# Kernel tuning notes

Measured on AMD Instinct MI355X. Metric: run time of the kernel, lower is better.

## Reference

```python
import jax, jax.numpy as jnp
import numpy as np
from jax import lax

LRELU_SLOPE = 0.2
GAIN = 2.0 ** 0.5
EPS = 1e-8


def setup_inputs() -> dict:
    key = jax.random.key(0)
    ks = jax.random.split(key, 8)
    B, NDW, CIN, COUT, H, W = 4, 512, 16, 16, 1024, 1024
    return {
        "w": jax.random.normal(ks[0], (B, NDW), jnp.float32),
        "x": jax.random.normal(ks[1], (B, CIN, H, W), jnp.float32),
        "noise": jax.random.normal(ks[2], (B, 1, H, W), jnp.float32),
        "fc_weight": jax.random.normal(ks[3], (CIN, NDW), jnp.float32),
        "fc_bias": jnp.ones((CIN,), jnp.float32),
        "conv_weight": jax.random.normal(ks[4], (COUT, CIN, 3, 3), jnp.float32),
        "conv_bias": jax.random.normal(ks[5], (COUT,), jnp.float32),
        "scale_noise": jnp.float32(0.1),
    }


def reference(w, x, noise, fc_weight, fc_bias, conv_weight, conv_bias, scale_noise):
    NDW = fc_weight.shape[1]
    COUT, CIN, KH, KW = conv_weight.shape
    # equal_lr scaling (FC): weight * n_dim_in**-0.5
    s = w @ (fc_weight.T * (NDW ** -0.5)) + fc_bias  # [B, CIN] style per input channel
    # equal_lr scaling (Conv): weight * (in_channels * k^2)**-0.5
    wc = conv_weight * ((CIN * KH * KW) ** -0.5)  # [COUT, CIN, 3, 3]
    # demodulation coefficient: d[b,o] = 1/sqrt(sum_{i,kh,kw} (s[b,i]*wc[o,i,kh,kw])^2 + eps)
    w2 = (wc ** 2).sum(axis=(2, 3))  # [COUT, CIN]
    d = lax.rsqrt((s ** 2) @ w2.T + EPS)  # [B, COUT]
    # modulate input instead of materializing per-sample weights (mathematically identical)
    xm = x * s[:, :, None, None]
    y = lax.conv_general_dilated(
        xm, wc, window_strides=(1, 1), padding=((1, 1), (1, 1)),
        dimension_numbers=("NCHW", "OIHW", "NCHW"))
    y = y * d[:, :, None, None] + conv_bias[None, :, None, None]
    y = y + scale_noise * noise  # broadcast noise over channels
    y = GAIN * jnp.where(y >= 0, y, LRELU_SLOPE * y)
    return (w, y)
```

## Files before the change

kernel.cpp:

```cpp
#include <hip/hip_runtime.h>

#define H_ 1024
#define W_ 1024
#define B_ 4
#define CIN 16
#define COUT 16
#define TH 8
#define TW 64
#define NT 16
#define ROWS 10
#define COLS_U 74

#define LRELU 0.2f
#define GAIN_ 1.4142135623730951f
#define EPS_ 1e-8f

#define BAR_LGKM()                                                      \
    do {                                                                \
        __builtin_amdgcn_sched_barrier(0);                              \
        asm volatile("s_waitcnt lgkmcnt(0)\n\ts_barrier" ::: "memory"); \
        __builtin_amdgcn_sched_barrier(0);                              \
    } while (0)

typedef __attribute__((ext_vector_type(8))) short bf16x8;
typedef __attribute__((ext_vector_type(16))) float f32x16;

static __device__ __forceinline__ unsigned short f32_to_bf16(float f) {
    unsigned int u = __float_as_uint(f);
    unsigned int r = u + 0x7FFF + ((u >> 16) & 1);
    return (unsigned short)(r >> 16);
}

static __device__ __forceinline__ float f4c(const float4& v, int px) {
    return px == 0 ? v.x : px == 1 ? v.y : px == 2 ? v.z : v.w;
}

static __device__ __forceinline__ int swz(int c) { return c + (c >> 3); }

__global__ __launch_bounds__(256) void k_setup1(
    const float* __restrict__ w, const float* __restrict__ fcw,
    const float* __restrict__ fcb, float* __restrict__ s_out,
    float* __restrict__ w_copy_out)
{
    __shared__ float part[256];
    const int tid = threadIdx.x;
    const int bi = tid >> 2;
    const int q  = tid & 3;
    const int b = bi >> 4, i = bi & 15;
    const float* wr = w + b * 512 + q * 128;
    const float* fr = fcw + i * 512 + q * 128;
    float acc = 0.f;
    #pragma unroll 8
    for (int k = 0; k < 128; ++k) acc += wr[k] * fr[k];
    part[tid] = acc;
    __syncthreads();
    if (tid < 64) {
        float v = part[tid*4] + part[tid*4+1] + part[tid*4+2] + part[tid*4+3];
        s_out[tid] = v * 0.04419417382415922f  + fcb[tid & 15];
    }
    for (int e = tid; e < B_ * 512; e += 256) w_copy_out[e] = w[e];
}

__global__ __launch_bounds__(256) void k_setup2(
    const float* __restrict__ s_in, const float* __restrict__ convw,
    unsigned short* __restrict__ afrag)
{
    const int b = blockIdx.x;
    const int tid = threadIdx.x;
    __shared__ float s_sh[16];
    __shared__ float d_sh[16];
    __shared__ float wc_sh[COUT * CIN * 9];
    __shared__ float part[256];

    if (tid < 16) s_sh[tid] = s_in[b * 16 + tid];
    for (int e = tid; e < COUT * CIN * 9; e += 256)
        wc_sh[e] = convw[e] * (1.0f / 12.0f);
    __syncthreads();

    const int o = tid >> 4, i = tid & 15;
    const float si = s_sh[i];
    float acc = 0.f;
    #pragma unroll
    for (int tap = 0; tap < 9; ++tap) {
        float v = wc_sh[(o * 16 + i) * 9 + tap] * si;
        acc += v * v;
    }
    part[tid] = acc;
    __syncthreads();
    if (tid < 16) {
        float sum = EPS_;
        #pragma unroll
        for (int j = 0; j < 16; ++j) sum += part[tid * 16 + j];
        d_sh[tid] = rsqrtf(sum);
    }
    __syncthreads();

    for (int e = tid; e < 6 * 64 * 8; e += 256) {
        const int f    = e >> 9;
        const int lane = (e >> 3) & 63;
        const int j    = e & 7;
        const int C    = (f < 3) ? f : (f - 3);
        const bool isQ = (f >= 3);
        const int oo = lane & 15;
        const int R  = (lane >> 4) & 1;
        const int ii = 8 * (lane >> 5) + j;
        int tap;
        if (!isQ) tap = 3 * R + C;
        else      tap = (R == 0) ? (6 + C) : -1;
        float v = 0.f;
        if (tap >= 0) v = wc_sh[(oo * 16 + ii) * 9 + tap] * s_sh[ii] * d_sh[oo];
        afrag[(size_t)b * (6 * 64 * 8) + e] = f32_to_bf16(v);
    }
}

__global__ __launch_bounds__(320) void k_conv(
    const float* __restrict__ x, const float* __restrict__ noise,
    const float* __restrict__ conv_bias, const float* __restrict__ sn_ptr,
    const unsigned short* __restrict__ afrag, float* __restrict__ y)
{
    __shared__ unsigned short tile[2][ROWS][COLS_U][8];

    const int tid = threadIdx.x;
    const int bt = blockIdx.z;
    const int h0s = blockIdx.y * (TH * NT);
    const int w0 = blockIdx.x * TW;
    const float sn = sn_ptr[0];
    const float* xb = x + (size_t)bt * CIN * H_ * W_;
    float* yb = y + (size_t)bt * COUT * H_ * W_;
    const float* nb = noise + (size_t)bt * H_ * W_;

    const int lane = tid & 63;
    const int wid  = tid >> 6;

    const int rowS = tid >> 5;
    const int subS = tid & 31;
    const int hhS  = subS >> 4;
    const int cgS  = subS & 15;
    const bool hasE = (tid >= 256) && (tid < 296);
    const int e_   = tid - 256;
    const int rowE = e_ >> 2, sideE = (e_ >> 1) & 1, hhE = e_ & 1;

    float4 vS[8];
    float  ev[8];

    auto stage_load = [&](int t) {
        const int gh0 = h0s + TH * t - 1;
        {
            const int gh = gh0 + rowS;
            const bool ok = (gh >= 0) && (gh < H_);
            const float* base = xb + ((size_t)(8 * hhS) * H_ + gh) * W_ + (w0 + 4 * cgS);
            #pragma unroll
            for (int c = 0; c < 8; ++c) {
                vS[c] = make_float4(0.f, 0.f, 0.f, 0.f);
                if (ok) vS[c] = *reinterpret_cast<const float4*>(base + (size_t)c * H_ * W_);
            }
        }
        if (hasE) {
            const int gh = gh0 + rowE;
            const int gw = w0 - 1 + sideE * 65;
            const bool ok = (gh >= 0) && (gh < H_) && (gw >= 0) && (gw < W_);
            #pragma unroll
            for (int c = 0; c < 8; ++c)
                ev[c] = ok ? xb[((size_t)(8 * hhE + c) * H_ + gh) * W_ + gw] : 0.f;
        }
    };

    auto stage_write = [&]() {
        #pragma unroll
        for (int px = 0; px < 4; ++px) {
            bf16x8 pk;
            #pragma unroll
            for (int c = 0; c < 8; ++c) pk[c] = (short)f32_to_bf16(f4c(vS[c], px));
            const int u = swz(1 + 4 * cgS + px);
            *reinterpret_cast<bf16x8*>(&tile[hhS][rowS][u][0]) = pk;
        }
        if (hasE) {
            bf16x8 pk;
            #pragma unroll
            for (int c = 0; c < 8; ++c) pk[c] = (short)f32_to_bf16(ev[c]);
            const int u = sideE ? swz(65) : 0;
            *reinterpret_cast<bf16x8*>(&tile[hhE][rowE][u][0]) = pk;
        }
    };

    const int s_ = wid & 1;
    const int g_ = (wid >> 1) & 1;
    const int baseRow = 4 * s_;
    const int colBase = g_ * 32 + (lane & 31);
    const int chalfB  = lane >> 5;

    bf16x8 aP[3], aQ[3];
    {
        const bf16x8* ap = reinterpret_cast<const bf16x8*>(afrag + (size_t)bt * 6 * 64 * 8);
        #pragma unroll
        for (int C = 0; C < 3; ++C) {
            aP[C] = ap[C * 64 + lane];
            aQ[C] = ap[(3 + C) * 64 + lane];
        }
    }
    int   o_j[8];
    float bias_j[8];
    #pragma unroll
    for (int j = 0; j < 8; ++j) {
        o_j[j] = (j & 3) + 8 * (j >> 2) + 4 * chalfB;
        bias_j[j] = conv_bias[o_j[j]];
    }

    auto compute = [&](int t) {
        if (wid >= 4) return;
        const int ghBase = h0s + TH * t + 4 * s_;
        f32x16 zro;
        #pragma unroll
        for (int i = 0; i < 16; ++i) zro[i] = 0.f;
        f32x16 cacc[5];
        #pragma unroll
        for (int k = 0; k < 6; ++k) {
            bf16x8 bv0, bv1, bv2;
            {
                const unsigned short* rbase = &tile[chalfB][baseRow + k][0][0];
                const int c0 = colBase,     u0 = swz(c0);
                const int c1 = colBase + 1, u1 = swz(c1);
                const int c2 = colBase + 2, u2 = swz(c2);
                bv0 = *reinterpret_cast<const bf16x8*>(&rbase[u0 * 8]);
                bv1 = *reinterpret_cast<const bf16x8*>(&rbase[u1 * 8]);
                bv2 = *reinterpret_cast<const bf16x8*>(&rbase[u2 * 8]);
            }
            if (k <= 4) {
                f32x16 t0 = __builtin_amdgcn_mfma_f32_32x32x16_bf16(aP[0], bv0, zro, 0, 0, 0);
                t0 = __builtin_amdgcn_mfma_f32_32x32x16_bf16(aP[1], bv1, t0, 0, 0, 0);
                t0 = __builtin_amdgcn_mfma_f32_32x32x16_bf16(aP[2], bv2, t0, 0, 0, 0);
                cacc[k] = t0;
            }
            if (k >= 2) {
                f32x16 t1 = cacc[k - 2];
                t1 = __builtin_amdgcn_mfma_f32_32x32x16_bf16(aQ[0], bv0, t1, 0, 0, 0);
                t1 = __builtin_amdgcn_mfma_f32_32x32x16_bf16(aQ[1], bv1, t1, 0, 0, 0);
                t1 = __builtin_amdgcn_mfma_f32_32x32x16_bf16(aQ[2], bv2, t1, 0, 0, 0);
                cacc[k - 2] = t1;
                const int r = k - 2;
                const int gh = ghBase + r;
                const float noi = nb[(size_t)gh * W_ + w0 + colBase] * sn;
                #pragma unroll
                for (int j = 0; j < 8; ++j) {
                    float v = cacc[k - 2][j] + cacc[k - 1][8 + j] + bias_j[j] + noi;
                    v = (v >= 0.f) ? v : (LRELU * v);
                    yb[((size_t)o_j[j] * H_ + gh) * W_ + w0 + colBase] = v * GAIN_;
                }
            }
        }
    };

    stage_load(0);
    for (int t = 0; t < NT; ++t) {
        if (t > 0) BAR_LGKM();
        stage_write();
        BAR_LGKM();
        if (t + 1 < NT) stage_load(t + 1);
        compute(t);
    }
}

extern "C" void kernel_launch(void* const* d_in, const int* in_sizes, int n_in,
                              void* d_out, int out_size, void* d_ws, size_t ws_size,
                              hipStream_t stream)
{
    const float* w     = (const float*)d_in[0];
    const float* x     = (const float*)d_in[1];
    const float* noise = (const float*)d_in[2];
    const float* fcw   = (const float*)d_in[3];
    const float* fcb   = (const float*)d_in[4];
    const float* convw = (const float*)d_in[5];
    const float* convb = (const float*)d_in[6];
    const float* sn    = (const float*)d_in[7];

    float* out = (float*)d_out;
    float* ws_s = (float*)d_ws;
    unsigned short* ws_afrag = (unsigned short*)((char*)d_ws + 256);

    k_setup1<<<1, 256, 0, stream>>>(w, fcw, fcb, ws_s, out);
    k_setup2<<<B_, 256, 0, stream>>>(ws_s, convw, ws_afrag);
    dim3 grid(W_ / TW, H_ / (TH * NT), B_);
    k_conv<<<grid, 320, 0, stream>>>(x, noise, convb, sn, ws_afrag, out + 2048);
}
```

Measured before the change: 167.6 us.

## Prefetch noise rows early, rotate accumulators, and raise wave priority during MFMA compute

Noise values for the four output rows are now loaded at the start of each tile iteration, before the LDS stage write, so their latency overlaps the barrier and staging instead of stalling the epilogue. The compute loop is hand-unrolled with a three-register rotating accumulator set instead of a five-entry array, which shrinks register pressure. Compute waves raise their scheduling priority with s_setprio around the MFMA section. The cost is four extra live registers for noise and more code size.

```diff
diff --git a/kernel.cpp b/kernel.cpp
--- a/kernel.cpp
+++ b/kernel.cpp
@@ -142,6 +142,7 @@
 
     float4 vS[8];
     float  ev[8];
+    float  nv[4];
 
     auto stage_load = [&](int t) {
         const int gh0 = h0s + TH * t - 1;
@@ -165,29 +166,38 @@
         }
     };
 
-    auto stage_write = [&]() {
-        #pragma unroll
-        for (int px = 0; px < 4; ++px) {
-            bf16x8 pk;
-            #pragma unroll
-            for (int c = 0; c < 8; ++c) pk[c] = (short)f32_to_bf16(f4c(vS[c], px));
-            const int u = swz(1 + 4 * cgS + px);
-            *reinterpret_cast<bf16x8*>(&tile[hhS][rowS][u][0]) = pk;
-        }
-        if (hasE) {
-            bf16x8 pk;
-            #pragma unroll
-            for (int c = 0; c < 8; ++c) pk[c] = (short)f32_to_bf16(ev[c]);
-            const int u = sideE ? swz(65) : 0;
-            *reinterpret_cast<bf16x8*>(&tile[hhE][rowE][u][0]) = pk;
-        }
-    };
-
     const int s_ = wid & 1;
     const int g_ = (wid >> 1) & 1;
     const int baseRow = 4 * s_;
     const int colBase = g_ * 32 + (lane & 31);
     const int chalfB  = lane >> 5;
+
+    auto noise_prefetch = [&](int t) {
+        if (wid < 4) {
+            const int ghB = h0s + TH * t + 4 * s_;
+            #pragma unroll
+            for (int r = 0; r < 4; ++r)
+                nv[r] = nb[(size_t)(ghB + r) * W_ + w0 + colBase];
+        }
+    };
+
+    auto stage_write = [&]() {
+        #pragma unroll
+        for (int px = 0; px < 4; ++px) {
+            bf16x8 pk;
+            #pragma unroll
+            for (int c = 0; c < 8; ++c) pk[c] = (short)f32_to_bf16(f4c(vS[c], px));
+            const int u = swz(1 + 4 * cgS + px);
+            *reinterpret_cast<bf16x8*>(&tile[hhS][rowS][u][0]) = pk;
+        }
+        if (hasE) {
+            bf16x8 pk;
+            #pragma unroll
+            for (int c = 0; c < 8; ++c) pk[c] = (short)f32_to_bf16(ev[c]);
+            const int u = sideE ? swz(65) : 0;
+            *reinterpret_cast<bf16x8*>(&tile[hhE][rowE][u][0]) = pk;
+        }
+    };
 
     bf16x8 aP[3], aQ[3];
     {
@@ -206,53 +216,53 @@
         bias_j[j] = conv_bias[o_j[j]];
     }
 
+#define KROW(K, BORN, PREV, FIN)                                                     \
+    {                                                                                \
+        const unsigned short* rbase = &tile[chalfB][baseRow + (K)][0][0];            \
+        bf16x8 bv0 = *reinterpret_cast<const bf16x8*>(&rbase[swz(colBase + 0) * 8]); \
+        bf16x8 bv1 = *reinterpret_cast<const bf16x8*>(&rbase[swz(colBase + 1) * 8]); \
+        bf16x8 bv2 = *reinterpret_cast<const bf16x8*>(&rbase[swz(colBase + 2) * 8]); \
+        if ((K) <= 4) {                                                              \
+            _Pragma("unroll")                                                        \
+            for (int i_ = 0; i_ < 16; ++i_) BORN[i_] = 0.f;                          \
+            BORN = __builtin_amdgcn_mfma_f32_32x32x16_bf16(aP[0], bv0, BORN, 0, 0, 0); \
+            BORN = __builtin_amdgcn_mfma_f32_32x32x16_bf16(aP[1], bv1, BORN, 0, 0, 0); \
+            BORN = __builtin_amdgcn_mfma_f32_32x32x16_bf16(aP[2], bv2, BORN, 0, 0, 0); \
+        }                                                                            \
+        if ((K) >= 2) {                                                              \
+            FIN = __builtin_amdgcn_mfma_f32_32x32x16_bf16(aQ[0], bv0, FIN, 0, 0, 0); \
+            FIN = __builtin_amdgcn_mfma_f32_32x32x16_bf16(aQ[1], bv1, FIN, 0, 0, 0); \
+            FIN = __builtin_amdgcn_mfma_f32_32x32x16_bf16(aQ[2], bv2, FIN, 0, 0, 0); \
+            const int r_ = (K) - 2;                                                  \
+            const int gh_ = ghBase + r_;                                             \
+            const float noi_ = nv[r_] * sn;                                          \
+            _Pragma("unroll")                                                        \
+            for (int j_ = 0; j_ < 8; ++j_) {                                         \
+                float v_ = FIN[j_] + PREV[8 + j_] + bias_j[j_] + noi_;               \
+                v_ = (v_ >= 0.f) ? v_ : (LRELU * v_);                                \
+                yb[((size_t)o_j[j_] * H_ + gh_) * W_ + w0 + colBase] = v_ * GAIN_;   \
+            }                                                                        \
+        }                                                                            \
+    }
+
     auto compute = [&](int t) {
         if (wid >= 4) return;
         const int ghBase = h0s + TH * t + 4 * s_;
-        f32x16 zro;
-        #pragma unroll
-        for (int i = 0; i < 16; ++i) zro[i] = 0.f;
-        f32x16 cacc[5];
-        #pragma unroll
-        for (int k = 0; k < 6; ++k) {
-            bf16x8 bv0, bv1, bv2;
-            {
-                const unsigned short* rbase = &tile[chalfB][baseRow + k][0][0];
-                const int c0 = colBase,     u0 = swz(c0);
-                const int c1 = colBase + 1, u1 = swz(c1);
-                const int c2 = colBase + 2, u2 = swz(c2);
-                bv0 = *reinterpret_cast<const bf16x8*>(&rbase[u0 * 8]);
-                bv1 = *reinterpret_cast<const bf16x8*>(&rbase[u1 * 8]);
-                bv2 = *reinterpret_cast<const bf16x8*>(&rbase[u2 * 8]);
-            }
-            if (k <= 4) {
-                f32x16 t0 = __builtin_amdgcn_mfma_f32_32x32x16_bf16(aP[0], bv0, zro, 0, 0, 0);
-                t0 = __builtin_amdgcn_mfma_f32_32x32x16_bf16(aP[1], bv1, t0, 0, 0, 0);
-                t0 = __builtin_amdgcn_mfma_f32_32x32x16_bf16(aP[2], bv2, t0, 0, 0, 0);
-                cacc[k] = t0;
-            }
-            if (k >= 2) {
-                f32x16 t1 = cacc[k - 2];
-                t1 = __builtin_amdgcn_mfma_f32_32x32x16_bf16(aQ[0], bv0, t1, 0, 0, 0);
-                t1 = __builtin_amdgcn_mfma_f32_32x32x16_bf16(aQ[1], bv1, t1, 0, 0, 0);
-                t1 = __builtin_amdgcn_mfma_f32_32x32x16_bf16(aQ[2], bv2, t1, 0, 0, 0);
-                cacc[k - 2] = t1;
-                const int r = k - 2;
-                const int gh = ghBase + r;
-                const float noi = nb[(size_t)gh * W_ + w0 + colBase] * sn;
-                #pragma unroll
-                for (int j = 0; j < 8; ++j) {
-                    float v = cacc[k - 2][j] + cacc[k - 1][8 + j] + bias_j[j] + noi;
-                    v = (v >= 0.f) ? v : (LRELU * v);
-                    yb[((size_t)o_j[j] * H_ + gh) * W_ + w0 + colBase] = v * GAIN_;
-                }
-            }
-        }
+        f32x16 c0, c1, c2;
+        __builtin_amdgcn_s_setprio(1);
+        KROW(0, c0, c2, c1);
+        KROW(1, c1, c0, c2);
+        KROW(2, c2, c1, c0);
+        KROW(3, c0, c2, c1);
+        KROW(4, c1, c0, c2);
+        KROW(5, c2, c1, c0);
+        __builtin_amdgcn_s_setprio(0);
     };
 
     stage_load(0);
     for (int t = 0; t < NT; ++t) {
         if (t > 0) BAR_LGKM();
+        noise_prefetch(t);
         stage_write();
         BAR_LGKM();
         if (t + 1 < NT) stage_load(t + 1);
```

New measurement: 166.3 us (median of 2 runs). No clear change (-0.8%).
